# Kernel optimization log

Hardware: AMD Instinct MI355X
Metric: run time of the kernel (lower is better)

Reference implementation:

```python
import jax, jax.numpy as jnp
import numpy as np

N, VW, DW, VP, DP, H, M = 1024, 50000, 300, 50, 100, 512, 256


def _run_dir(x, Wih, Whh, b, reverse):
    # Single-direction LSTM over [n, in] -> [n, H]. PyTorch gate order i,f,g,o.
    Hh = Whh.shape[1]
    def step(carry, xt):
        h, c = carry
        z = xt @ Wih.T + h @ Whh.T + b  # [4H]
        i, f, g, o = jnp.split(z, 4, axis=-1)
        c = jax.nn.sigmoid(f) * c + jax.nn.sigmoid(i) * jnp.tanh(g)
        h = jax.nn.sigmoid(o) * jnp.tanh(c)
        return (h, c), h
    init = (jnp.zeros((Hh,), x.dtype), jnp.zeros((Hh,), x.dtype))
    _, hs = jax.lax.scan(step, init, x, reverse=reverse)
    return hs


def setup_inputs() -> dict:
    key = jax.random.key(0)
    ks = jax.random.split(key, 24)
    s = 0.05  # small init to keep tanh/sigmoid unsaturated
    d = {
        "word_idx": jax.random.randint(ks[0], (N,), 0, VW, dtype=jnp.int32),
        "pos_idx": jax.random.randint(ks[1], (N,), 0, VP, dtype=jnp.int32),
        "word_emb": jax.random.normal(ks[2], (VW, DW), jnp.float32) * s,
        "pos_emb": jax.random.normal(ks[3], (VP, DP), jnp.float32) * s,
        "wih0f": jax.random.normal(ks[4], (4 * H, DW + DP), jnp.float32) * s,
        "whh0f": jax.random.normal(ks[5], (4 * H, H), jnp.float32) * s,
        "b0f": jax.random.normal(ks[6], (4 * H,), jnp.float32) * s,
        "wih0r": jax.random.normal(ks[7], (4 * H, DW + DP), jnp.float32) * s,
        "whh0r": jax.random.normal(ks[8], (4 * H, H), jnp.float32) * s,
        "b0r": jax.random.normal(ks[9], (4 * H,), jnp.float32) * s,
        "wih1f": jax.random.normal(ks[10], (4 * H, 2 * H), jnp.float32) * s,
        "whh1f": jax.random.normal(ks[11], (4 * H, H), jnp.float32) * s,
        "b1f": jax.random.normal(ks[12], (4 * H,), jnp.float32) * s,
        "wih1r": jax.random.normal(ks[13], (4 * H, 2 * H), jnp.float32) * s,
        "whh1r": jax.random.normal(ks[14], (4 * H, H), jnp.float32) * s,
        "b1r": jax.random.normal(ks[15], (4 * H,), jnp.float32) * s,
        "W1": jax.random.normal(ks[16], (M, 4 * H), jnp.float32) * s,
        "bmlp1": jax.random.normal(ks[17], (M,), jnp.float32) * s,
        "w2": jax.random.normal(ks[18], (1, M), jnp.float32) * s,
        "b2": jax.random.normal(ks[19], (1,), jnp.float32) * s,
    }
    return d


def reference(word_idx, pos_idx, word_emb, pos_emb,
              wih0f, whh0f, b0f, wih0r, whh0r, b0r,
              wih1f, whh1f, b1f, wih1r, whh1r, b1r,
              W1, bmlp1, w2, b2):
    # Embed words + pos, concat -> [n, 400]
    x = jnp.concatenate([word_emb[word_idx], pos_emb[pos_idx]], axis=1)
    # 2-layer bidirectional LSTM encoder (batch of 1 squeezed away, as in the module)
    h0 = jnp.concatenate([_run_dir(x, wih0f, whh0f, b0f, False),
                          _run_dir(x, wih0r, whh0r, b0r, True)], axis=1)   # [n, 2H]
    h1 = jnp.concatenate([_run_dir(h0, wih1f, whh1f, b1f, False),
                          _run_dir(h0, wih1r, whh1r, b1r, True)], axis=1)  # [n, 2H]
    # Pairwise MLP score: MLP(concat(h_i, h_j)). Split W1 into head/dep halves so the
    # big GEMM is done once per token instead of once per pair (same math).
    twoH = h1.shape[1]
    a = h1 @ W1[:, :twoH].T            # [n, M], contribution of h_i
    bpart = h1 @ W1[:, twoH:].T        # [n, M], contribution of h_j
    hidden = jnp.tanh(a[:, None, :] + bpart[None, :, :] + bmlp1)  # [n, n, M]
    scores = hidden @ w2[0] + b2[0]    # [n, n]
    return scores
```

## Files before the change

kernel.cpp:

```cpp
#include <hip/hip_runtime.h>
#include <hip/hip_bf16.h>

#define HID   512
#define SEQ   1024
#define GATES 2048

__device__ __forceinline__ float sigm(float x) {
    return 1.f / (1.f + __expf(-x));
}
__device__ __forceinline__ float tanh_fast(float x) {
    float ax = fabsf(x);
    float e  = __expf(-2.f * ax);
    float t  = (1.f - e) * __builtin_amdgcn_rcpf(1.f + e);
    return copysignf(t, x);
}
__device__ __forceinline__ float bcast(float v, int l) {
    return __uint_as_float((unsigned)__builtin_amdgcn_readlane((int)__float_as_uint(v), l));
}

__global__ void embed_kernel(const int* __restrict__ wi, const int* __restrict__ pi,
                             const float* __restrict__ we, const float* __restrict__ pe,
                             float* __restrict__ x) {
    int i = blockIdx.x;
    int t = threadIdx.x;
    const float* w = we + (size_t)wi[i] * 300;
    const float* p = pe + (size_t)pi[i] * 100;
    float* xo = x + (size_t)i * 400;
    for (int c = t; c < 300; c += 128) xo[c]       = w[c];
    for (int c = t; c < 100; c += 128) xo[300 + c] = p[c];
}

__global__ __launch_bounds__(256)
void gemm_bias2(const float* __restrict__ A,
                const float* __restrict__ B0, const float* __restrict__ bias0, float* __restrict__ C0,
                const float* __restrict__ B1, const float* __restrict__ bias1, float* __restrict__ C1,
                int M, int N, int K, int lda, int ldb, int ldc) {
    const float* B    = blockIdx.z ? B1    : B0;
    const float* bias = blockIdx.z ? bias1 : bias0;
    float*       C    = blockIdx.z ? C1    : C0;

    __shared__ __align__(16) float As[16 * 132];
    __shared__ __align__(16) float Bs[16 * 68];
    const int tid  = threadIdx.x;
    const int bn   = blockIdx.x, bm = blockIdx.y;
    const int tj   = tid & 15, ti = tid >> 4;
    const int arow = tid >> 1;
    const int ak8  = (tid & 1) * 8;
    const int brow = tid >> 2;
    const int bk4  = (tid & 3) * 4;
    float acc[8][4] = {};

    for (int kt = 0; kt < K; kt += 16) {
        float4 a0 = *(const float4*)(A + (size_t)(bm * 128 + arow) * lda + kt + ak8);
        float4 a1 = *(const float4*)(A + (size_t)(bm * 128 + arow) * lda + kt + ak8 + 4);
        float4 bv = *(const float4*)(B + (size_t)(bn * 64 + brow) * ldb + kt + bk4);
        As[(ak8 + 0) * 132 + arow] = a0.x; As[(ak8 + 1) * 132 + arow] = a0.y;
        As[(ak8 + 2) * 132 + arow] = a0.z; As[(ak8 + 3) * 132 + arow] = a0.w;
        As[(ak8 + 4) * 132 + arow] = a1.x; As[(ak8 + 5) * 132 + arow] = a1.y;
        As[(ak8 + 6) * 132 + arow] = a1.z; As[(ak8 + 7) * 132 + arow] = a1.w;
        Bs[(bk4 + 0) * 68 + brow] = bv.x; Bs[(bk4 + 1) * 68 + brow] = bv.y;
        Bs[(bk4 + 2) * 68 + brow] = bv.z; Bs[(bk4 + 3) * 68 + brow] = bv.w;
        __syncthreads();
        #pragma unroll
        for (int k = 0; k < 16; ++k) {
            float4 x0 = *(const float4*)&As[k * 132 + ti * 8];
            float4 x1 = *(const float4*)&As[k * 132 + ti * 8 + 4];
            float4 b4 = *(const float4*)&Bs[k * 68 + tj * 4];
            const float av[8] = {x0.x, x0.y, x0.z, x0.w, x1.x, x1.y, x1.z, x1.w};
            #pragma unroll
            for (int i = 0; i < 8; ++i) {
                acc[i][0] = fmaf(av[i], b4.x, acc[i][0]);
                acc[i][1] = fmaf(av[i], b4.y, acc[i][1]);
                acc[i][2] = fmaf(av[i], b4.z, acc[i][2]);
                acc[i][3] = fmaf(av[i], b4.w, acc[i][3]);
            }
        }
        __syncthreads();
    }
    const int n0 = bn * 64 + tj * 4;
    float bb0 = 0.f, bb1 = 0.f, bb2 = 0.f, bb3 = 0.f;
    if (bias) { bb0 = bias[n0]; bb1 = bias[n0 + 1]; bb2 = bias[n0 + 2]; bb3 = bias[n0 + 3]; }
    #pragma unroll
    for (int i = 0; i < 8; ++i) {
        float4 o;
        o.x = acc[i][0] + bb0; o.y = acc[i][1] + bb1;
        o.z = acc[i][2] + bb2; o.w = acc[i][3] + bb3;
        *(float4*)(C + (size_t)(bm * 128 + ti * 8 + i) * ldc + n0) = o;
    }
}

__global__ __launch_bounds__(576)
void lstm_layer(const float* __restrict__ Zf, const float* __restrict__ Zr,
                const float* __restrict__ WhhF, const float* __restrict__ WhhR,
                unsigned long long* __restrict__ Hpair,
                float* __restrict__ Hout,
                unsigned tagBase) {
    const int dir = blockIdx.x >> 5;
    const int wg  = blockIdx.x & 31;
    const float* __restrict__ Z   = dir ? Zr   : Zf;
    const float* __restrict__ Whh = dir ? WhhR : WhhF;
    const int colOff = dir ? HID : 0;

    const int tid  = threadIdx.x;
    const int wave = tid >> 6;
    const int lane = tid & 63;
    const int g    = lane >> 4;
    const int jj   = lane & 15;
    const int grow = g * HID + wg * 16 + jj;

    __shared__ float part[2][8 * 65];

    if (wave == 0) {
        float cval = 0.f;
        float zin = Z[(size_t)(dir ? (SEQ - 1) : 0) * GATES + grow];
        for (int s = 0; s < SEQ; ++s) {
            const int t = dir ? (SEQ - 1 - s) : s;
            float znxt = 0.f;
            if (s + 1 < SEQ) {
                const int tn = dir ? (SEQ - 2 - s) : (s + 1);
                znxt = Z[(size_t)tn * GATES + grow];
            }
            __syncthreads();
            const float* pp = part[s & 1];
            float r = zin;
            #pragma unroll
            for (int c = 0; c < 8; ++c) r += pp[c * 65 + lane];
            float nl = (g == 2) ? tanh_fast(r) : sigm(r);
            float ig = __shfl(nl, jj);
            float fg = __shfl(nl, 16 + jj);
            float gg = __shfl(nl, 32 + jj);
            float og = __shfl(nl, 48 + jj);
            if (lane < 16) {
                cval = fg * cval + ig * gg;
                float hv = og * tanh_fast(cval);
                const size_t oidx = (size_t)t * (2 * HID) + colOff + wg * 16 + lane;
                unsigned long long pk = ((unsigned long long)(tagBase + (unsigned)s) << 32)
                                      | (unsigned long long)__float_as_uint(hv);
                __hip_atomic_store(Hpair + oidx, pk, __ATOMIC_RELAXED, __HIP_MEMORY_SCOPE_AGENT);
                Hout[oidx] = hv;
            }
            zin = znxt;
        }
    } else {
        const int kc = wave - 1;
        float w[64];
        {
            const float4* wp = (const float4*)(Whh + (size_t)grow * HID + kc * 64);
            #pragma unroll
            for (int q = 0; q < 16; ++q) {
                float4 v = wp[q];
                w[4 * q] = v.x; w[4 * q + 1] = v.y; w[4 * q + 2] = v.z; w[4 * q + 3] = v.w;
            }
        }
        for (int s = 0; s < SEQ; ++s) {
            const int t = dir ? (SEQ - 1 - s) : s;
            float acc = 0.f;
            if (s > 0) {
                const int tp = dir ? (t + 1) : (t - 1);
                const unsigned expTag = tagBase + (unsigned)s - 1u;
                const unsigned long long* hp =
                    Hpair + (size_t)tp * (2 * HID) + colOff + kc * 64 + lane;
                unsigned long long va, vb, v;
                va = __hip_atomic_load(hp, __ATOMIC_RELAXED, __HIP_MEMORY_SCOPE_AGENT);
                for (;;) {
                    vb = __hip_atomic_load(hp, __ATOMIC_RELAXED, __HIP_MEMORY_SCOPE_AGENT);
                    if (__all((unsigned)(va >> 32) == expTag)) { v = va; break; }
                    va = __hip_atomic_load(hp, __ATOMIC_RELAXED, __HIP_MEMORY_SCOPE_AGENT);
                    if (__all((unsigned)(vb >> 32) == expTag)) { v = vb; break; }
                }
                float hv = __uint_as_float((unsigned)v);
                float a0 = 0.f, a1 = 0.f, a2 = 0.f, a3 = 0.f;
                #pragma unroll
                for (int m = 0; m < 64; m += 4) {
                    a0 = fmaf(w[m + 0], bcast(hv, m + 0), a0);
                    a1 = fmaf(w[m + 1], bcast(hv, m + 1), a1);
                    a2 = fmaf(w[m + 2], bcast(hv, m + 2), a2);
                    a3 = fmaf(w[m + 3], bcast(hv, m + 3), a3);
                }
                acc = (a0 + a1) + (a2 + a3);
            }
            part[s & 1][kc * 65 + lane] = acc;
            __syncthreads();
        }
    }
}

__global__ __launch_bounds__(256)
void pairwise_kernel(const float* __restrict__ Ah, const float* __restrict__ Bd,
                     const float* __restrict__ w2, const float* __restrict__ b2,
                     float* __restrict__ out) {
    __shared__ __align__(16) float at[16 * 260];
    __shared__ __align__(16) float bt[16 * 260];
    __shared__ __align__(16) float wl[256];
    const int tid = threadIdx.x;
    const int i0 = blockIdx.y * 16, j0 = blockIdx.x * 16;
    for (int u = tid; u < 16 * 256; u += 256) {
        int r = u >> 8, m = u & 255;
        at[r * 260 + m] = Ah[(size_t)(i0 + r) * 256 + m];
        bt[r * 260 + m] = Bd[(size_t)(j0 + r) * 256 + m];
    }
    wl[tid] = w2[tid];
    __syncthreads();
    const int tj = tid & 15, ti = tid >> 4;
    float acc = b2[0];
    #pragma unroll 2
    for (int m = 0; m < 256; m += 4) {
        float4 a4 = *(const float4*)&at[ti * 260 + m];
        float4 b4 = *(const float4*)&bt[tj * 260 + m];
        float4 w4 = *(const float4*)&wl[m];
        acc += tanh_fast(a4.x + b4.x) * w4.x;
        acc += tanh_fast(a4.y + b4.y) * w4.y;
        acc += tanh_fast(a4.z + b4.z) * w4.z;
        acc += tanh_fast(a4.w + b4.w) * w4.w;
    }
    out[(size_t)(i0 + ti) * 1024 + (j0 + tj)] = acc;
}

extern "C" void kernel_launch(void* const* d_in, const int* in_sizes, int n_in,
                              void* d_out, int out_size, void* d_ws, size_t ws_size,
                              hipStream_t stream) {
    const int*   wi    = (const int*)  d_in[0];
    const int*   pi    = (const int*)  d_in[1];
    const float* we    = (const float*)d_in[2];
    const float* pe    = (const float*)d_in[3];
    const float* wih0f = (const float*)d_in[4];
    const float* whh0f = (const float*)d_in[5];
    const float* b0f   = (const float*)d_in[6];
    const float* wih0r = (const float*)d_in[7];
    const float* whh0r = (const float*)d_in[8];
    const float* b0r   = (const float*)d_in[9];
    const float* wih1f = (const float*)d_in[10];
    const float* whh1f = (const float*)d_in[11];
    const float* b1f   = (const float*)d_in[12];
    const float* wih1r = (const float*)d_in[13];
    const float* whh1r = (const float*)d_in[14];
    const float* b1r   = (const float*)d_in[15];
    const float* W1    = (const float*)d_in[16];
    const float* bmlp1 = (const float*)d_in[17];
    const float* w2    = (const float*)d_in[18];
    const float* b2    = (const float*)d_in[19];
    float* out = (float*)d_out;

    char* wsb = (char*)d_ws;
    float* x  = (float*)(wsb + 512);
    float* zA = x  + (size_t)1024 * 400;
    float* zB = zA + (size_t)1024 * 2048;
    float* h0 = zB + (size_t)1024 * 2048;
    float* h1 = h0 + (size_t)1024 * 1024;
    float* aH = h1 + (size_t)1024 * 1024;
    float* bD = aH + (size_t)1024 * 256;
    unsigned long long* Hpair = (unsigned long long*)(bD + (size_t)1024 * 256);

    embed_kernel<<<dim3(1024), dim3(128), 0, stream>>>(wi, pi, we, pe, x);

    gemm_bias2<<<dim3(32, 8, 2), dim3(256), 0, stream>>>(
        x, wih0f, b0f, zA, wih0r, b0r, zB, 1024, 2048, 400, 400, 400, 2048);

    lstm_layer<<<dim3(64), dim3(576), 0, stream>>>(zA, zB, whh0f, whh0r, Hpair, h0, 1u);

    gemm_bias2<<<dim3(32, 8, 2), dim3(256), 0, stream>>>(
        h0, wih1f, b1f, zA, wih1r, b1r, zB, 1024, 2048, 1024, 1024, 1024, 2048);

    lstm_layer<<<dim3(64), dim3(576), 0, stream>>>(zA, zB, whh1f, whh1r, Hpair, h1, 8192u);

    gemm_bias2<<<dim3(4, 8, 2), dim3(256), 0, stream>>>(
        h1, W1, bmlp1, aH, W1 + 1024, nullptr, bD, 1024, 256, 1024, 1024, 2048, 256);

    pairwise_kernel<<<dim3(64, 64), dim3(256), 0, stream>>>(aH, bD, w2, b2, out);
}
```

Measured before the change: 3.392 ms.

## Fuse input-projection GEMM into LSTM kernel with per-tile readiness counters

Each LSTM layer launch now also runs the input-projection GEMM on 192 extra blocks. Those blocks compute 128-row tiles in the order the forward and reverse recurrences need them and signal completion through per-row-block atomic counters. The recurrent waves spin on the counter before reading each new 128-timestep chunk of Z. This overlaps the GEMM with the serial recurrence and removes a kernel launch per layer. In exchange it relies on all 256 blocks being co-resident to avoid deadlock, and the GEMM blocks compete with the LSTM blocks for CUs.

Result: slower. 3.510 ms (+3.5%).

```diff
diff --git a/kernel.cpp b/kernel.cpp
--- a/kernel.cpp
+++ b/kernel.cpp
@@ -17,10 +17,14 @@
 __device__ __forceinline__ float bcast(float v, int l) {
     return __uint_as_float((unsigned)__builtin_amdgcn_readlane((int)__float_as_uint(v), l));
 }
+__device__ __forceinline__ void wait_tiles32(const unsigned* c) {
+    while (__hip_atomic_load(c, __ATOMIC_ACQUIRE, __HIP_MEMORY_SCOPE_AGENT) != 32u) {}
+}
 
 __global__ void embed_kernel(const int* __restrict__ wi, const int* __restrict__ pi,
                              const float* __restrict__ we, const float* __restrict__ pe,
-                             float* __restrict__ x) {
+                             float* __restrict__ x, unsigned* __restrict__ cnt) {
+    if (blockIdx.x == 0 && threadIdx.x < 32) cnt[threadIdx.x] = 0u;
     int i = blockIdx.x;
     int t = threadIdx.x;
     const float* w = we + (size_t)wi[i] * 300;
@@ -90,34 +94,116 @@
 }
 
 __global__ __launch_bounds__(576)
-void lstm_layer(const float* __restrict__ Zf, const float* __restrict__ Zr,
+void lstm_fused(const float* __restrict__ Zf, const float* __restrict__ Zr,
                 const float* __restrict__ WhhF, const float* __restrict__ WhhR,
                 unsigned long long* __restrict__ Hpair,
                 float* __restrict__ Hout,
-                unsigned tagBase) {
-    const int dir = blockIdx.x >> 5;
-    const int wg  = blockIdx.x & 31;
+                unsigned tagBase,
+                const float* __restrict__ Ag,
+                const float* __restrict__ Bg0, const float* __restrict__ bg0, float* __restrict__ Cg0,
+                const float* __restrict__ Bg1, const float* __restrict__ bg1, float* __restrict__ Cg1,
+                int K, int ldab,
+                unsigned* __restrict__ cnt) {
+    __shared__ __align__(16) float As[16 * 132];
+    __shared__ __align__(16) float Bs[16 * 68];
+    __shared__ float part[2][8 * 65];
+
+    const int b   = blockIdx.x;
+    const int tid = threadIdx.x;
+
+    if (b >= 64) {
+        const int gb  = b - 64;
+        const bool act = tid < 256;
+        const int tj   = tid & 15, ti = tid >> 4;
+        const int arow = tid >> 1;
+        const int ak8  = (tid & 1) * 8;
+        const int brow = tid >> 2;
+        const int bk4  = (tid & 3) * 4;
+        for (int o = gb; o < 512; o += 192) {
+            const int level = o >> 6;
+            const int half  = (o >> 5) & 1;
+            const int bn    = o & 31;
+            const int bz    = half;
+            const int bm    = half ? (7 - level) : level;
+            const float* Bm   = bz ? Bg1 : Bg0;
+            const float* bias = bz ? bg1 : bg0;
+            float*       C    = bz ? Cg1 : Cg0;
+            float acc[8][4] = {};
+            for (int kt = 0; kt < K; kt += 16) {
+                if (act) {
+                    float4 a0 = *(const float4*)(Ag + (size_t)(bm * 128 + arow) * ldab + kt + ak8);
+                    float4 a1 = *(const float4*)(Ag + (size_t)(bm * 128 + arow) * ldab + kt + ak8 + 4);
+                    float4 bv = *(const float4*)(Bm + (size_t)(bn * 64 + brow) * ldab + kt + bk4);
+                    As[(ak8 + 0) * 132 + arow] = a0.x; As[(ak8 + 1) * 132 + arow] = a0.y;
+                    As[(ak8 + 2) * 132 + arow] = a0.z; As[(ak8 + 3) * 132 + arow] = a0.w;
+                    As[(ak8 + 4) * 132 + arow] = a1.x; As[(ak8 + 5) * 132 + arow] = a1.y;
+                    As[(ak8 + 6) * 132 + arow] = a1.z; As[(ak8 + 7) * 132 + arow] = a1.w;
+                    Bs[(bk4 + 0) * 68 + brow] = bv.x; Bs[(bk4 + 1) * 68 + brow] = bv.y;
+                    Bs[(bk4 + 2) * 68 + brow] = bv.z; Bs[(bk4 + 3) * 68 + brow] = bv.w;
+                }
+                __syncthreads();
+                if (act) {
+                    #pragma unroll
+                    for (int k = 0; k < 16; ++k) {
+                        float4 x0 = *(const float4*)&As[k * 132 + ti * 8];
+                        float4 x1 = *(const float4*)&As[k * 132 + ti * 8 + 4];
+                        float4 b4 = *(const float4*)&Bs[k * 68 + tj * 4];
+                        const float av[8] = {x0.x, x0.y, x0.z, x0.w, x1.x, x1.y, x1.z, x1.w};
+                        #pragma unroll
+                        for (int i = 0; i < 8; ++i) {
+                            acc[i][0] = fmaf(av[i], b4.x, acc[i][0]);
+                            acc[i][1] = fmaf(av[i], b4.y, acc[i][1]);
+                            acc[i][2] = fmaf(av[i], b4.z, acc[i][2]);
+                            acc[i][3] = fmaf(av[i], b4.w, acc[i][3]);
+                        }
+                    }
+                }
+                __syncthreads();
+            }
+            if (act) {
+                const int n0 = bn * 64 + tj * 4;
+                float bb0 = 0.f, bb1 = 0.f, bb2 = 0.f, bb3 = 0.f;
+                if (bias) { bb0 = bias[n0]; bb1 = bias[n0 + 1]; bb2 = bias[n0 + 2]; bb3 = bias[n0 + 3]; }
+                #pragma unroll
+                for (int i = 0; i < 8; ++i) {
+                    float4 ov;
+                    ov.x = acc[i][0] + bb0; ov.y = acc[i][1] + bb1;
+                    ov.z = acc[i][2] + bb2; ov.w = acc[i][3] + bb3;
+                    *(float4*)(C + (size_t)(bm * 128 + ti * 8 + i) * 2048 + n0) = ov;
+                }
+            }
+            __syncthreads();
+            if (tid == 0)
+                __hip_atomic_fetch_add(&cnt[bz * 8 + bm], 1u,
+                                       __ATOMIC_RELEASE, __HIP_MEMORY_SCOPE_AGENT);
+        }
+        return;
+    }
+
+    const int dir = b >> 5;
+    const int wg  = b & 31;
     const float* __restrict__ Z   = dir ? Zr   : Zf;
     const float* __restrict__ Whh = dir ? WhhR : WhhF;
     const int colOff = dir ? HID : 0;
 
-    const int tid  = threadIdx.x;
     const int wave = tid >> 6;
     const int lane = tid & 63;
     const int g    = lane >> 4;
     const int jj   = lane & 15;
     const int grow = g * HID + wg * 16 + jj;
 
-    __shared__ float part[2][8 * 65];
-
     if (wave == 0) {
+        const unsigned* zcnt = cnt + dir * 8;
         float cval = 0.f;
-        float zin = Z[(size_t)(dir ? (SEQ - 1) : 0) * GATES + grow];
+        const int t0 = dir ? (SEQ - 1) : 0;
+        wait_tiles32(zcnt + (t0 >> 7));
+        float zin = Z[(size_t)t0 * GATES + grow];
         for (int s = 0; s < SEQ; ++s) {
             const int t = dir ? (SEQ - 1 - s) : s;
             float znxt = 0.f;
             if (s + 1 < SEQ) {
                 const int tn = dir ? (SEQ - 2 - s) : (s + 1);
+                if ((tn & 127) == (dir ? 127 : 0)) wait_tiles32(zcnt + (tn >> 7));
                 znxt = Z[(size_t)tn * GATES + grow];
             }
             __syncthreads();
@@ -242,6 +328,7 @@
     float* out = (float*)d_out;
 
     char* wsb = (char*)d_ws;
+    unsigned* cnt = (unsigned*)wsb;
     float* x  = (float*)(wsb + 512);
     float* zA = x  + (size_t)1024 * 400;
     float* zB = zA + (size_t)1024 * 2048;
@@ -251,17 +338,15 @@
     float* bD = aH + (size_t)1024 * 256;
     unsigned long long* Hpair = (unsigned long long*)(bD + (size_t)1024 * 256);
 
-    embed_kernel<<<dim3(1024), dim3(128), 0, stream>>>(wi, pi, we, pe, x);
-
-    gemm_bias2<<<dim3(32, 8, 2), dim3(256), 0, stream>>>(
-        x, wih0f, b0f, zA, wih0r, b0r, zB, 1024, 2048, 400, 400, 400, 2048);
-
-    lstm_layer<<<dim3(64), dim3(576), 0, stream>>>(zA, zB, whh0f, whh0r, Hpair, h0, 1u);
-
-    gemm_bias2<<<dim3(32, 8, 2), dim3(256), 0, stream>>>(
-        h0, wih1f, b1f, zA, wih1r, b1r, zB, 1024, 2048, 1024, 1024, 1024, 2048);
-
-    lstm_layer<<<dim3(64), dim3(576), 0, stream>>>(zA, zB, whh1f, whh1r, Hpair, h1, 8192u);
+    embed_kernel<<<dim3(1024), dim3(128), 0, stream>>>(wi, pi, we, pe, x, cnt);
+
+    lstm_fused<<<dim3(256), dim3(576), 0, stream>>>(
+        zA, zB, whh0f, whh0r, Hpair, h0, 1u,
+        x, wih0f, b0f, zA, wih0r, b0r, zB, 400, 400, cnt);
+
+    lstm_fused<<<dim3(256), dim3(576), 0, stream>>>(
+        zA, zB, whh1f, whh1r, Hpair, h1, 8192u,
+        h0, wih1f, b1f, zA, wih1r, b1r, zB, 1024, 1024, cnt + 16);
 
     gemm_bias2<<<dim3(4, 8, 2), dim3(256), 0, stream>>>(
         h1, W1, bmlp1, aH, W1 + 1024, nullptr, bD, 1024, 256, 1024, 1024, 2048, 256);
```

## Publish gate activations instead of h and recompute cell state in consumer waves

Applied to the files above, without the earlier changes.

The LSTM producer wave now publishes the tagged nonlinear gate values to global memory before the cross-lane shuffles and cell update, instead of publishing h afterwards. Each consumer wave polls the four gates for its 64-column slice, keeps a redundant copy of the cell state and recomputes h locally. This shortens the critical path between blocks by taking the cell update off it. In exchange each consumer issues four times as many polling loads per step, every block computes the cell update redundantly, and a zeroing pass over a larger flag buffer is added to the embed kernel.

Result: slower. 4.673 ms (+37.8%).

```diff
diff --git a/kernel.cpp b/kernel.cpp
--- a/kernel.cpp
+++ b/kernel.cpp
@@ -20,7 +20,10 @@
 
 __global__ void embed_kernel(const int* __restrict__ wi, const int* __restrict__ pi,
                              const float* __restrict__ we, const float* __restrict__ pe,
-                             float* __restrict__ x) {
+                             float* __restrict__ x, unsigned long long* __restrict__ Hgate) {
+    size_t gtid = (size_t)blockIdx.x * 128 + threadIdx.x;
+    for (size_t k = gtid; k < (size_t)SEQ * 2 * GATES; k += (size_t)1024 * 128)
+        Hgate[k] = 0ull;
     int i = blockIdx.x;
     int t = threadIdx.x;
     const float* w = we + (size_t)wi[i] * 300;
@@ -92,7 +95,7 @@
 __global__ __launch_bounds__(576)
 void lstm_layer(const float* __restrict__ Zf, const float* __restrict__ Zr,
                 const float* __restrict__ WhhF, const float* __restrict__ WhhR,
-                unsigned long long* __restrict__ Hpair,
+                unsigned long long* __restrict__ Hgate,
                 float* __restrict__ Hout,
                 unsigned tagBase) {
     const int dir = blockIdx.x >> 5;
@@ -126,18 +129,18 @@
             #pragma unroll
             for (int c = 0; c < 8; ++c) r += pp[c * 65 + lane];
             float nl = (g == 2) ? tanh_fast(r) : sigm(r);
+            unsigned long long pk = ((unsigned long long)(tagBase + (unsigned)s) << 32)
+                                  | (unsigned long long)__float_as_uint(nl);
+            __hip_atomic_store(Hgate + ((size_t)t * 2 + dir) * GATES + grow, pk,
+                               __ATOMIC_RELAXED, __HIP_MEMORY_SCOPE_AGENT);
             float ig = __shfl(nl, jj);
             float fg = __shfl(nl, 16 + jj);
             float gg = __shfl(nl, 32 + jj);
             float og = __shfl(nl, 48 + jj);
             if (lane < 16) {
-                cval = fg * cval + ig * gg;
+                cval = fmaf(fg, cval, ig * gg);
                 float hv = og * tanh_fast(cval);
-                const size_t oidx = (size_t)t * (2 * HID) + colOff + wg * 16 + lane;
-                unsigned long long pk = ((unsigned long long)(tagBase + (unsigned)s) << 32)
-                                      | (unsigned long long)__float_as_uint(hv);
-                __hip_atomic_store(Hpair + oidx, pk, __ATOMIC_RELAXED, __HIP_MEMORY_SCOPE_AGENT);
-                Hout[oidx] = hv;
+                Hout[(size_t)t * (2 * HID) + colOff + wg * 16 + lane] = hv;
             }
             zin = znxt;
         }
@@ -152,23 +155,37 @@
                 w[4 * q] = v.x; w[4 * q + 1] = v.y; w[4 * q + 2] = v.z; w[4 * q + 3] = v.w;
             }
         }
+        float ccell = 0.f;
         for (int s = 0; s < SEQ; ++s) {
             const int t = dir ? (SEQ - 1 - s) : s;
             float acc = 0.f;
             if (s > 0) {
                 const int tp = dir ? (t + 1) : (t - 1);
                 const unsigned expTag = tagBase + (unsigned)s - 1u;
-                const unsigned long long* hp =
-                    Hpair + (size_t)tp * (2 * HID) + colOff + kc * 64 + lane;
-                unsigned long long va, vb, v;
-                va = __hip_atomic_load(hp, __ATOMIC_RELAXED, __HIP_MEMORY_SCOPE_AGENT);
+                const unsigned long long* gp =
+                    Hgate + ((size_t)tp * 2 + dir) * GATES + kc * 64 + lane;
+                #define LDG(o) __hip_atomic_load(gp + (o), __ATOMIC_RELAXED, __HIP_MEMORY_SCOPE_AGENT)
+                #define OKT(x) ((unsigned)((x) >> 32) == expTag)
+                unsigned long long ia, fa, ga, oa, ib, fb, gb, ob, vi, vf, vg, vo;
+                ia = LDG(0); fa = LDG(512); ga = LDG(1024); oa = LDG(1536);
                 for (;;) {
-                    vb = __hip_atomic_load(hp, __ATOMIC_RELAXED, __HIP_MEMORY_SCOPE_AGENT);
-                    if (__all((unsigned)(va >> 32) == expTag)) { v = va; break; }
-                    va = __hip_atomic_load(hp, __ATOMIC_RELAXED, __HIP_MEMORY_SCOPE_AGENT);
-                    if (__all((unsigned)(vb >> 32) == expTag)) { v = vb; break; }
+                    ib = LDG(0); fb = LDG(512); gb = LDG(1024); ob = LDG(1536);
+                    if (__all(OKT(ia) & OKT(fa) & OKT(ga) & OKT(oa))) {
+                        vi = ia; vf = fa; vg = ga; vo = oa; break;
+                    }
+                    ia = LDG(0); fa = LDG(512); ga = LDG(1024); oa = LDG(1536);
+                    if (__all(OKT(ib) & OKT(fb) & OKT(gb) & OKT(ob))) {
+                        vi = ib; vf = fb; vg = gb; vo = ob; break;
+                    }
                 }
-                float hv = __uint_as_float((unsigned)v);
+                #undef LDG
+                #undef OKT
+                float iv = __uint_as_float((unsigned)vi);
+                float fv = __uint_as_float((unsigned)vf);
+                float gv = __uint_as_float((unsigned)vg);
+                float ov = __uint_as_float((unsigned)vo);
+                ccell = fmaf(fv, ccell, iv * gv);
+                float hv = ov * tanh_fast(ccell);
                 float a0 = 0.f, a1 = 0.f, a2 = 0.f, a3 = 0.f;
                 #pragma unroll
                 for (int m = 0; m < 64; m += 4) {
@@ -249,19 +266,19 @@
     float* h1 = h0 + (size_t)1024 * 1024;
     float* aH = h1 + (size_t)1024 * 1024;
     float* bD = aH + (size_t)1024 * 256;
-    unsigned long long* Hpair = (unsigned long long*)(bD + (size_t)1024 * 256);
-
-    embed_kernel<<<dim3(1024), dim3(128), 0, stream>>>(wi, pi, we, pe, x);
+    unsigned long long* Hgate = (unsigned long long*)(bD + (size_t)1024 * 256);
+
+    embed_kernel<<<dim3(1024), dim3(128), 0, stream>>>(wi, pi, we, pe, x, Hgate);
 
     gemm_bias2<<<dim3(32, 8, 2), dim3(256), 0, stream>>>(
         x, wih0f, b0f, zA, wih0r, b0r, zB, 1024, 2048, 400, 400, 400, 2048);
 
-    lstm_layer<<<dim3(64), dim3(576), 0, stream>>>(zA, zB, whh0f, whh0r, Hpair, h0, 1u);
+    lstm_layer<<<dim3(64), dim3(576), 0, stream>>>(zA, zB, whh0f, whh0r, Hgate, h0, 1u);
 
     gemm_bias2<<<dim3(32, 8, 2), dim3(256), 0, stream>>>(
         h0, wih1f, b1f, zA, wih1r, b1r, zB, 1024, 2048, 1024, 1024, 1024, 2048);
 
-    lstm_layer<<<dim3(64), dim3(576), 0, stream>>>(zA, zB, whh1f, whh1r, Hpair, h1, 8192u);
+    lstm_layer<<<dim3(64), dim3(576), 0, stream>>>(zA, zB, whh1f, whh1r, Hgate, h1, 8192u);
 
     gemm_bias2<<<dim3(4, 8, 2), dim3(256), 0, stream>>>(
         h1, W1, bmlp1, aH, W1 + 1024, nullptr, bD, 1024, 256, 1024, 1024, 2048, 256);
```
